# Kernel tuning notes

Hardware: AMD Instinct MI355X
Metric: run time of the kernel (lower is better)

The kernel has to match this reference:

```python
import jax, jax.numpy as jnp
import numpy as np
from jax import lax

RENDER_SIZE = (228, 304)   # (H, W) from __init__ default
FAR = 100.0                # z-buffer init, matches depth_map fill in source
EPS = 1e-7
CHUNK = 128                # faces processed per scan step


def setup_inputs() -> dict:
    key = jax.random.key(0)
    k1, k2, k3 = jax.random.split(key, 3)
    B, N, M = 1, 8192, 2048
    H, W = RENDER_SIZE
    uv = jax.random.uniform(k1, (B, N, 2), dtype=jnp.float32)           # u,v in [0,1]
    d = jax.random.uniform(k2, (B, N, 1), dtype=jnp.float32) * 4.0 + 1.0  # depth in [1,5]
    verts = jnp.concatenate([uv, d], axis=-1)                            # [B,N,3] depthmap format
    faces = jax.random.randint(k3, (B, M, 3), 0, N)                      # [B,M,3]
    fx = fy = 260.0
    K = jnp.array([[fx, 0.0, W / 2.0], [0.0, fy, H / 2.0], [0.0, 0.0, 1.0]], jnp.float32)
    intrinsics = jnp.tile(K[None], (B, 1, 1))
    ang = 0.02  # small camera rotation about y
    R = jnp.array([[np.cos(ang), 0.0, np.sin(ang)], [0.0, 1.0, 0.0],
                   [-np.sin(ang), 0.0, np.cos(ang)]], jnp.float32)
    R_mat = jnp.tile(R[None], (B, 1, 1))
    t_mat = jnp.tile(jnp.array([[0.01], [0.0], [0.02]], jnp.float32)[None], (B, 1, 1))
    return {"verts": verts, "faces": faces, "intrinsics": intrinsics,
            "R_mat": R_mat, "t_mat": t_mat}


def _convert_depthmap_to_cam(verts, K, H, W):
    # depthmap (u,v,d) -> camera coords; mirrors convert_depthmap_to_cam
    d = verts[..., 2:3]
    pix = jnp.concatenate([verts[..., 0:1] * W, verts[..., 1:2] * H,
                           jnp.ones_like(d)], axis=-1)                   # [B,N,3]
    Kinv = jnp.linalg.inv(K)
    return jnp.einsum('bij,bnj->bni', Kinv, pix) * d


def _project_cam_to_depthmap(cam, K, H, W):
    # camera coords -> depthmap (u,v,z); mirrors project_cam_to_depthmap
    z = cam[..., 2]
    p = jnp.stack([cam[..., 0] / (z + EPS), cam[..., 1] / (z + EPS),
                   jnp.ones_like(z)], axis=-1)
    p = jnp.einsum('bnj,bij->bni', p, K)  # matmul(p, K^T)
    u = jnp.clip(p[..., 0] / W, 0.0, 1.0)
    v = jnp.clip(p[..., 1] / H, 0.0, 1.0)
    return jnp.stack([u, v, z], axis=-1)


def _transform_depthmap(verts, K, R, t, H, W):
    cam = _convert_depthmap_to_cam(verts, K, H, W)                       # [B,N,3]
    cam2 = jnp.einsum('bij,bnj->bni', R, cam) + t[:, :, 0][:, None, :]   # R@x + t
    return _project_cam_to_depthmap(cam2, K, H, W)


def _rasterize(face_verts, S):
    """face_verts: [B,M,3,3] NDC (x,y) + depth z. Returns depth [B,S,S], sil [B,S,S]."""
    B, M = face_verts.shape[0], face_verts.shape[1]
    p = (2.0 * jnp.arange(S, dtype=face_verts.dtype) + 1.0 - S) / S      # NR pixel centers
    XP = p[None, None, None, :]   # x varies along last axis
    YP = p[None, None, :, None]   # y varies along rows

    chunks = face_verts.reshape(B, M // CHUNK, CHUNK, 3, 3).transpose(1, 0, 2, 3, 4)

    def step(carry, fvc):  # fvc: [B,C,3,3]
        depth, sil = carry
        x = fvc[..., 0][..., None, None]  # [B,C,3,1,1]
        y = fvc[..., 1][..., None, None]
        z = fvc[..., 2][..., None, None]
        x0, x1, x2 = x[:, :, 0], x[:, :, 1], x[:, :, 2]
        y0, y1, y2 = y[:, :, 0], y[:, :, 1], y[:, :, 2]
        z0, z1, z2 = z[:, :, 0], z[:, :, 1], z[:, :, 2]
        denom = (y1 - y2) * (x0 - x2) + (x2 - x1) * (y0 - y2)
        ok = jnp.abs(denom) > 1e-10
        safe = jnp.where(ok, denom, 1.0)
        w0 = ((y1 - y2) * (XP - x2) + (x2 - x1) * (YP - y2)) / safe      # [B,C,S,S]
        w1 = ((y2 - y0) * (XP - x2) + (x0 - x2) * (YP - y2)) / safe
        w2 = 1.0 - w0 - w1
        inside = (w0 >= 0) & (w1 >= 0) & (w2 >= 0) & ok
        inv_z = w0 / z0 + w1 / z1 + w2 / z2  # perspective-correct depth interp
        zp = 1.0 / jnp.where(jnp.abs(inv_z) > EPS, inv_z, EPS)
        zc = jnp.where(inside & (zp > 0), zp, FAR)
        depth = jnp.minimum(depth, zc.min(axis=1))                       # z-buffer update
        sil = jnp.maximum(sil, inside.any(axis=1).astype(depth.dtype))
        return (depth, sil), None

    init = (jnp.full((B, S, S), FAR, face_verts.dtype),
            jnp.zeros((B, S, S), face_verts.dtype))
    (depth, sil), _ = lax.scan(step, init, chunks)
    return depth, sil


def reference(verts, faces, intrinsics, R_mat, t_mat):
    H, W = RENDER_SIZE
    S = max(H, W)
    v = _transform_depthmap(verts, intrinsics, R_mat, t_mat, H, W)       # reprojected depthmap
    # depthmap [0,1] -> NDC [-1,1], keeping aspect via img_max_size
    ndc = jnp.concatenate([v[:, :, :1] * W / S * 2.0 - 1.0,
                           v[:, :, 1:2] * H / S * 2.0 - 1.0,
                           v[:, :, 2:]], axis=2)
    fv = jax.vmap(lambda vb, fb: vb[fb])(ndc, faces)                     # [B,M,3,3]
    depth, sil = _rasterize(fv, S)
    depth = depth[:, ::-1, :][:, :H, :W]  # flip(dim=1) then crop, as in _render
    sil = sil[:, ::-1, :][:, :H, :W]
    return jnp.stack([depth, sil], axis=1)  # [B,2,H,W]: depth + silhouette
```

## Files before the change

### kernel.cpp

```cpp
#include <hip/hip_runtime.h>

#define SS 304
#define HH 228
#define WW 304
#define FARV 100.0f
#define EPSV 1e-07f
#define SPLIT 16
#define CH 128

__device__ __forceinline__ void xform_vertex(
    float u, float v, float d,
    float fx, float cx, float fy, float cy,
    float r00, float r01, float r02,
    float r10, float r11, float r12,
    float r20, float r21, float r22,
    float t0, float t1, float t2,
    float& xn, float& yn, float& z)
{
#pragma clang fp contract(off)
    float ki00 = 1.0f / fx;
    float ki02 = -(cx / fx);
    float ki11 = 1.0f / fy;
    float ki12 = -(cy / fy);
    float px = u * (float)WW;
    float py = v * (float)HH;
    float c0 = (ki00 * px + ki02) * d;
    float c1 = (ki11 * py + ki12) * d;
    float c2 = d;
    float e0 = ((r00*c0 + r01*c1) + r02*c2) + t0;
    float e1 = ((r10*c0 + r11*c1) + r12*c2) + t1;
    float e2 = ((r20*c0 + r21*c1) + r22*c2) + t2;
    z = e2;
    float zd = z + EPSV;
    float p0 = e0 / zd;
    float p1 = e1 / zd;
    float q0 = p0 * fx + cx;
    float q1 = p1 * fy + cy;
    float uu = q0 / (float)WW; uu = fminf(fmaxf(uu, 0.0f), 1.0f);
    float vv = q1 / (float)HH; vv = fminf(fmaxf(vv, 0.0f), 1.0f);
    xn = uu * (float)WW / (float)SS * 2.0f - 1.0f;
    yn = vv * (float)HH / (float)SS * 2.0f - 1.0f;
}

__global__ __launch_bounds__(256) void prep_kernel(
    const float* __restrict__ verts,
    const int* __restrict__ faces,
    const float* __restrict__ Km,
    const float* __restrict__ Rm,
    const float* __restrict__ tm,
    float4* __restrict__ bboxArr,
    float4* __restrict__ G0arr,
    float4* __restrict__ G1arr,
    float2* __restrict__ G2arr,
    float* __restrict__ out, int M)
{
#pragma clang fp contract(off)
    int g = blockIdx.x * blockDim.x + threadIdx.x;
    if (g < HH * WW) {
        out[g] = FARV;
        out[HH * WW + g] = 0.0f;
    }
    if (g >= M) return;
    int m = g;
    int i0 = faces[3*m+0], i1 = faces[3*m+1], i2 = faces[3*m+2];
    float fx = Km[0], cx = Km[2], fy = Km[4], cy = Km[5];
    float r00 = Rm[0], r01 = Rm[1], r02 = Rm[2];
    float r10 = Rm[3], r11 = Rm[4], r12 = Rm[5];
    float r20 = Rm[6], r21 = Rm[7], r22 = Rm[8];
    float t0 = tm[0], t1 = tm[1], t2 = tm[2];

    float x0, y0, z0, x1, y1, z1, x2, y2, z2;
    xform_vertex(verts[3*i0+0], verts[3*i0+1], verts[3*i0+2], fx,cx,fy,cy,
                 r00,r01,r02,r10,r11,r12,r20,r21,r22,t0,t1,t2, x0,y0,z0);
    xform_vertex(verts[3*i1+0], verts[3*i1+1], verts[3*i1+2], fx,cx,fy,cy,
                 r00,r01,r02,r10,r11,r12,r20,r21,r22,t0,t1,t2, x1,y1,z1);
    xform_vertex(verts[3*i2+0], verts[3*i2+1], verts[3*i2+2], fx,cx,fy,cy,
                 r00,r01,r02,r10,r11,r12,r20,r21,r22,t0,t1,t2, x2,y2,z2);

    float A0 = y1 - y2;
    float B0 = x2 - x1;
    float A1 = y2 - y0;
    float B1 = x0 - x2;
    float dy02 = y0 - y2;
    float denom = A0 * B1 + B0 * dy02;
    bool ok = fabsf(denom) > 1e-10f;

    float xmin, xmax, ymin, ymax;
    if (ok) {
        xmin = fminf(x0, fminf(x1, x2)) - 1e-4f;
        xmax = fmaxf(x0, fmaxf(x1, x2)) + 1e-4f;
        ymin = fminf(y0, fminf(y1, y2)) - 1e-4f;
        ymax = fmaxf(y0, fmaxf(y1, y2)) + 1e-4f;
    } else {
        xmin = 1e30f; xmax = -1e30f; ymin = 1e30f; ymax = -1e30f;
    }
    bboxArr[m] = make_float4(xmin, xmax, ymin, ymax);

    float flip = (denom >= 0.0f) ? 1.0f : -1.0f;
    float sabs = fabsf(denom);
    float A0p = flip * A0, B0p = flip * B0;
    float C0p = -(A0p * x2 + B0p * y2);
    float A1p = flip * A1, B1p = flip * B1;
    float C1p = -(A1p * x2 + B1p * y2);
    float rz0 = 1.0f / z0, rz1 = 1.0f / z1, rz2 = 1.0f / z2;
    float D0 = rz0 / sabs, D1 = rz1 / sabs, D2 = rz2 / sabs;
    float d02 = D0 - D2, d12 = D1 - D2;
    float E = A0p * d02 + A1p * d12;
    float F = B0p * d02 + B1p * d12;
    float G = (C0p * d02 + C1p * d12) + sabs * D2;

    G0arr[m] = make_float4(A0p, B0p, C0p, sabs);
    G1arr[m] = make_float4(A1p, B1p, C1p, G);
    G2arr[m] = make_float2(E, F);
}

__global__ __launch_bounds__(256) void raster_kernel(
    const float4* __restrict__ bboxArr,
    const float4* __restrict__ G0arr,
    const float4* __restrict__ G1arr,
    const float2* __restrict__ G2arr,
    float* __restrict__ out, int M)
{
    __shared__ float4 sG0[CH];
    __shared__ float4 sG1[CH];
    __shared__ float2 sG2[CH];
    __shared__ int sCount;

    int tx = threadIdx.x, ty = threadIdx.y;
    int tid = ty * 16 + tx;
    int w = blockIdx.x * 16 + tx;
    int h = blockIdx.y * 16 + ty;

    int wlo = blockIdx.x * 16;
    int whi = min(wlo + 15, WW - 1);
    int hlo = blockIdx.y * 16;
    int hhi = min(hlo + 15, HH - 1);
    float txlo = ((float)(2*wlo + 1 - SS)) / (float)SS;
    float txhi = ((float)(2*whi + 1 - SS)) / (float)SS;
    float tylo = ((float)(2*(SS-1-hhi) + 1 - SS)) / (float)SS;
    float tyhi = ((float)(2*(SS-1-hlo) + 1 - SS)) / (float)SS;

    if (tid == 0) sCount = 0;
    __syncthreads();

    if (tid < CH) {
        int m = blockIdx.z * CH + tid;
        float4 rb = bboxArr[m];
        bool pass = !(rb.x > txhi || rb.y < txlo || rb.z > tyhi || rb.w < tylo);
        if (pass) {
            int i = atomicAdd(&sCount, 1);
            sG0[i] = G0arr[m];
            sG1[i] = G1arr[m];
            sG2[i] = G2arr[m];
        }
    }
    __syncthreads();
    int cnt = sCount;

    if (h < HH) {
        int irow = SS - 1 - h;
        float XP = ((float)(2*w    + 1 - SS)) / (float)SS;
        float YP = ((float)(2*irow + 1 - SS)) / (float)SS;

        float mx = 0.0f;

        for (int k = 0; k < cnt; ++k) {
            float4 g0 = sG0[k];
            float4 g1 = sG1[k];
            float2 g2 = sG2[k];
            float n0 = fmaf(g0.x, XP, fmaf(g0.y, YP, g0.z));
            float n1 = fmaf(g1.x, XP, fmaf(g1.y, YP, g1.z));
            float n2 = (g0.w - n0) - n1;
            float iz = fmaf(g2.x, XP, fmaf(g2.y, YP, g1.w));
            float m3 = fminf(fminf(n0, n1), n2);
            float cand = (m3 >= 0.0f) ? iz : 0.0f;
            mx = fmaxf(mx, cand);
        }

        if (mx > 0.0f) {
            float depth = __builtin_amdgcn_rcpf(mx);
            atomicMin((unsigned int*)&out[h * WW + w], __float_as_uint(depth));
            atomicMax((unsigned int*)&out[HH * WW + h * WW + w],
                      __float_as_uint(1.0f));
        }
    }
}

extern "C" void kernel_launch(void* const* d_in, const int* in_sizes, int n_in,
                              void* d_out, int out_size, void* d_ws, size_t ws_size,
                              hipStream_t stream) {
    const float* verts = (const float*)d_in[0];
    const int*   faces = (const int*)d_in[1];
    const float* K     = (const float*)d_in[2];
    const float* R     = (const float*)d_in[3];
    const float* t     = (const float*)d_in[4];
    float* out = (float*)d_out;

    int M = in_sizes[1] / 3;

    char* ws = (char*)d_ws;
    float4* bbox = (float4*)ws;                ws += (size_t)M * sizeof(float4);
    float4* G0   = (float4*)ws;                ws += (size_t)M * sizeof(float4);
    float4* G1   = (float4*)ws;                ws += (size_t)M * sizeof(float4);
    float2* G2   = (float2*)ws;                ws += (size_t)M * sizeof(float2);

    prep_kernel<<<(HH * WW + 255) / 256, 256, 0, stream>>>(
        verts, faces, K, R, t, bbox, G0, G1, G2, out, M);

    dim3 blk(16, 16);
    dim3 grd((WW + 15) / 16, (HH + 15) / 16, SPLIT);
    raster_kernel<<<grd, blk, 0, stream>>>(bbox, G0, G1, G2, out, M);
}
```

Measured before the change: 89.76 us.

## Rasterize two rows per thread and double faces per block chunk

Each thread now evaluates two pixels 16 rows apart, getting the second pixel's edge functions incrementally from the first with one FMA each. This amortizes the shared-memory face loads over two pixels. The face chunk grows to 256 with half as many splits, so all 256 threads take part in culling, and an M bound check is added. The trade-off is a bounding box twice as tall, so more faces pass culling per tile and more lanes can go idle, plus fewer blocks in the grid, which lowers occupancy.

```diff
diff --git a/kernel.cpp b/kernel.cpp
--- a/kernel.cpp
+++ b/kernel.cpp
@@ -5,8 +5,9 @@
 #define WW 304
 #define FARV 100.0f
 #define EPSV 1e-07f
-#define SPLIT 16
-#define CH 128
+#define SPLIT 8
+#define CH 256
+#define DYC (-32.0f / (float)SS)
 
 __device__ __forceinline__ void xform_vertex(
     float u, float v, float d,
@@ -128,13 +129,14 @@
 
     int tx = threadIdx.x, ty = threadIdx.y;
     int tid = ty * 16 + tx;
-    int w = blockIdx.x * 16 + tx;
-    int h = blockIdx.y * 16 + ty;
+    int w  = blockIdx.x * 16 + tx;
+    int h0 = blockIdx.y * 32 + ty;
+    int h1 = h0 + 16;
 
     int wlo = blockIdx.x * 16;
     int whi = min(wlo + 15, WW - 1);
-    int hlo = blockIdx.y * 16;
-    int hhi = min(hlo + 15, HH - 1);
+    int hlo = blockIdx.y * 32;
+    int hhi = min(hlo + 31, HH - 1);
     float txlo = ((float)(2*wlo + 1 - SS)) / (float)SS;
     float txhi = ((float)(2*whi + 1 - SS)) / (float)SS;
     float tylo = ((float)(2*(SS-1-hhi) + 1 - SS)) / (float)SS;
@@ -143,26 +145,29 @@
     if (tid == 0) sCount = 0;
     __syncthreads();
 
-    if (tid < CH) {
+    {
         int m = blockIdx.z * CH + tid;
-        float4 rb = bboxArr[m];
-        bool pass = !(rb.x > txhi || rb.y < txlo || rb.z > tyhi || rb.w < tylo);
-        if (pass) {
-            int i = atomicAdd(&sCount, 1);
-            sG0[i] = G0arr[m];
-            sG1[i] = G1arr[m];
-            sG2[i] = G2arr[m];
+        if (m < M) {
+            float4 rb = bboxArr[m];
+            bool pass = !(rb.x > txhi || rb.y < txlo || rb.z > tyhi || rb.w < tylo);
+            if (pass) {
+                int i = atomicAdd(&sCount, 1);
+                sG0[i] = G0arr[m];
+                sG1[i] = G1arr[m];
+                sG2[i] = G2arr[m];
+            }
         }
     }
     __syncthreads();
     int cnt = sCount;
 
-    if (h < HH) {
-        int irow = SS - 1 - h;
+    {
+        int irow = SS - 1 - h0;
         float XP = ((float)(2*w    + 1 - SS)) / (float)SS;
         float YP = ((float)(2*irow + 1 - SS)) / (float)SS;
 
-        float mx = 0.0f;
+        float mx0 = 0.0f;
+        float mx1 = 0.0f;
 
         for (int k = 0; k < cnt; ++k) {
             float4 g0 = sG0[k];
@@ -170,17 +175,28 @@
             float2 g2 = sG2[k];
             float n0 = fmaf(g0.x, XP, fmaf(g0.y, YP, g0.z));
             float n1 = fmaf(g1.x, XP, fmaf(g1.y, YP, g1.z));
+            float iz = fmaf(g2.x, XP, fmaf(g2.y, YP, g1.w));
             float n2 = (g0.w - n0) - n1;
-            float iz = fmaf(g2.x, XP, fmaf(g2.y, YP, g1.w));
             float m3 = fminf(fminf(n0, n1), n2);
-            float cand = (m3 >= 0.0f) ? iz : 0.0f;
-            mx = fmaxf(mx, cand);
-        }
-
-        if (mx > 0.0f) {
-            float depth = __builtin_amdgcn_rcpf(mx);
-            atomicMin((unsigned int*)&out[h * WW + w], __float_as_uint(depth));
-            atomicMax((unsigned int*)&out[HH * WW + h * WW + w],
+            mx0 = fmaxf(mx0, (m3 >= 0.0f) ? iz : 0.0f);
+            float n0b = fmaf(g0.y, DYC, n0);
+            float n1b = fmaf(g1.y, DYC, n1);
+            float izb = fmaf(g2.y, DYC, iz);
+            float n2b = (g0.w - n0b) - n1b;
+            float m3b = fminf(fminf(n0b, n1b), n2b);
+            mx1 = fmaxf(mx1, (m3b >= 0.0f) ? izb : 0.0f);
+        }
+
+        if (h0 < HH && mx0 > 0.0f) {
+            float depth = __builtin_amdgcn_rcpf(mx0);
+            atomicMin((unsigned int*)&out[h0 * WW + w], __float_as_uint(depth));
+            atomicMax((unsigned int*)&out[HH * WW + h0 * WW + w],
+                      __float_as_uint(1.0f));
+        }
+        if (h1 < HH && mx1 > 0.0f) {
+            float depth = __builtin_amdgcn_rcpf(mx1);
+            atomicMin((unsigned int*)&out[h1 * WW + w], __float_as_uint(depth));
+            atomicMax((unsigned int*)&out[HH * WW + h1 * WW + w],
                       __float_as_uint(1.0f));
         }
     }
@@ -208,6 +224,6 @@
         verts, faces, K, R, t, bbox, G0, G1, G2, out, M);
 
     dim3 blk(16, 16);
-    dim3 grd((WW + 15) / 16, (HH + 15) / 16, SPLIT);
+    dim3 grd((WW + 15) / 16, (HH + 31) / 32, SPLIT);
     raster_kernel<<<grd, blk, 0, stream>>>(bbox, G0, G1, G2, out, M);
 }
```

Result: faster. 81.38 us (-9.3%).

## Replace face-split raster grid with per-tile full loop, double-buffered staging

Applied to the files above, without the earlier changes.

Each 16x16 pixel tile now loops over all faces in batches of 256 instead of splitting faces across 16 z-blocks, so each pixel is written once directly and the global atomics and output init pass go away. Face culling adds an exact edge-function test against the tile corners, and compaction uses wave ballot plus one shared atomic per wave. Shared staging is double-buffered so the next batch is culled while the current one is rasterized. In exchange the grid shrinks to about 285 blocks, which lowers parallelism on a large GPU, and each block now does serial work over every face.

```diff
diff --git a/kernel.cpp b/kernel.cpp
--- a/kernel.cpp
+++ b/kernel.cpp
@@ -5,8 +5,6 @@
 #define WW 304
 #define FARV 100.0f
 #define EPSV 1e-07f
-#define SPLIT 16
-#define CH 128
 
 __device__ __forceinline__ void xform_vertex(
     float u, float v, float d,
@@ -51,17 +49,11 @@
     float4* __restrict__ bboxArr,
     float4* __restrict__ G0arr,
     float4* __restrict__ G1arr,
-    float2* __restrict__ G2arr,
-    float* __restrict__ out, int M)
+    float2* __restrict__ G2arr, int M)
 {
 #pragma clang fp contract(off)
-    int g = blockIdx.x * blockDim.x + threadIdx.x;
-    if (g < HH * WW) {
-        out[g] = FARV;
-        out[HH * WW + g] = 0.0f;
-    }
-    if (g >= M) return;
-    int m = g;
+    int m = blockIdx.x * blockDim.x + threadIdx.x;
+    if (m >= M) return;
     int i0 = faces[3*m+0], i1 = faces[3*m+1], i2 = faces[3*m+2];
     float fx = Km[0], cx = Km[2], fy = Km[4], cy = Km[5];
     float r00 = Rm[0], r01 = Rm[1], r02 = Rm[2];
@@ -121,68 +113,95 @@
     const float2* __restrict__ G2arr,
     float* __restrict__ out, int M)
 {
-    __shared__ float4 sG0[CH];
-    __shared__ float4 sG1[CH];
-    __shared__ float2 sG2[CH];
-    __shared__ int sCount;
-
-    int tx = threadIdx.x, ty = threadIdx.y;
-    int tid = ty * 16 + tx;
-    int w = blockIdx.x * 16 + tx;
-    int h = blockIdx.y * 16 + ty;
-
-    int wlo = blockIdx.x * 16;
-    int whi = min(wlo + 15, WW - 1);
-    int hlo = blockIdx.y * 16;
-    int hhi = min(hlo + 15, HH - 1);
-    float txlo = ((float)(2*wlo + 1 - SS)) / (float)SS;
-    float txhi = ((float)(2*whi + 1 - SS)) / (float)SS;
-    float tylo = ((float)(2*(SS-1-hhi) + 1 - SS)) / (float)SS;
-    float tyhi = ((float)(2*(SS-1-hlo) + 1 - SS)) / (float)SS;
-
-    if (tid == 0) sCount = 0;
+    __shared__ float4 sG0[2][256];
+    __shared__ float4 sG1[2][256];
+    __shared__ float2 sG2[2][256];
+    __shared__ int sCnt[2];
+
+    const int tx = threadIdx.x, ty = threadIdx.y;
+    const int tid = ty * 16 + tx;
+    const int w = blockIdx.x * 16 + tx;
+    const int h = blockIdx.y * 16 + ty;
+
+    const int wlo = blockIdx.x * 16, whi = wlo + 15;
+    const int hlo = blockIdx.y * 16, hhi = min(hlo + 15, HH - 1);
+    const float txlo = ((float)(2*wlo + 1 - SS)) / (float)SS;
+    const float txhi = ((float)(2*whi + 1 - SS)) / (float)SS;
+    const float tylo = ((float)(2*(SS-1-hhi) + 1 - SS)) / (float)SS;
+    const float tyhi = ((float)(2*(SS-1-hlo) + 1 - SS)) / (float)SS;
+
+    const int lane = tid & 63;
+    const unsigned long long lanes_below = (1ull << lane) - 1ull;
+
+    auto stage = [&](int b, int slot) {
+        int m = b * 256 + tid;
+        bool pass = false;
+        float4 g0, g1;
+        if (m < M) {
+            float4 rb = bboxArr[m];
+            if (!(rb.x > txhi || rb.y < txlo || rb.z > tyhi || rb.w < tylo)) {
+                g0 = G0arr[m];
+                g1 = G1arr[m];
+                float e0 = fmaxf(g0.x * txlo, g0.x * txhi)
+                         + fmaxf(g0.y * tylo, g0.y * tyhi) + g0.z;
+                float e1 = fmaxf(g1.x * txlo, g1.x * txhi)
+                         + fmaxf(g1.y * tylo, g1.y * tyhi) + g1.z;
+                float A2 = -(g0.x + g1.x);
+                float B2 = -(g0.y + g1.y);
+                float C2 = g0.w - g0.z - g1.z;
+                float e2 = fmaxf(A2 * txlo, A2 * txhi)
+                         + fmaxf(B2 * tylo, B2 * tyhi) + C2;
+                pass = (e0 >= -1e-5f) && (e1 >= -1e-5f) && (e2 >= -1e-5f);
+            }
+        }
+        unsigned long long mask = __ballot(pass);
+        int wtotal = __popcll(mask);
+        int wbase = 0;
+        if (lane == 0 && wtotal > 0) wbase = atomicAdd(&sCnt[slot], wtotal);
+        wbase = __shfl(wbase, 0);
+        if (pass) {
+            int i = wbase + (int)__popcll(mask & lanes_below);
+            sG0[slot][i] = g0;
+            sG1[slot][i] = g1;
+            sG2[slot][i] = G2arr[m];
+        }
+    };
+
+    if (tid < 2) sCnt[tid] = 0;
     __syncthreads();
-
-    if (tid < CH) {
-        int m = blockIdx.z * CH + tid;
-        float4 rb = bboxArr[m];
-        bool pass = !(rb.x > txhi || rb.y < txlo || rb.z > tyhi || rb.w < tylo);
-        if (pass) {
-            int i = atomicAdd(&sCount, 1);
-            sG0[i] = G0arr[m];
-            sG1[i] = G1arr[m];
-            sG2[i] = G2arr[m];
+    stage(0, 0);
+
+    const int irow = SS - 1 - h;
+    const float XP = ((float)(2*w    + 1 - SS)) / (float)SS;
+    const float YP = ((float)(2*irow + 1 - SS)) / (float)SS;
+    float mx = 0.0f;
+
+    const int nb = (M + 255) >> 8;
+    for (int b = 0; b < nb; ++b) {
+        int cur = b & 1, nxt = cur ^ 1;
+        __syncthreads();
+        int cnt = sCnt[cur];
+        __syncthreads();
+        if (tid == 0) sCnt[cur] = 0;
+        if (b + 1 < nb) stage(b + 1, nxt);
+        for (int k = 0; k < cnt; ++k) {
+            float4 g0 = sG0[cur][k];
+            float4 g1 = sG1[cur][k];
+            float2 g2 = sG2[cur][k];
+            float n0 = fmaf(g0.x, XP, fmaf(g0.y, YP, g0.z));
+            float n1 = fmaf(g1.x, XP, fmaf(g1.y, YP, g1.z));
+            float iz = fmaf(g2.x, XP, fmaf(g2.y, YP, g1.w));
+            float n2 = (g0.w - n0) - n1;
+            float m3 = fminf(fminf(n0, n1), n2);
+            mx = fmaxf(mx, (m3 >= 0.0f) ? iz : 0.0f);
         }
     }
-    __syncthreads();
-    int cnt = sCount;
 
     if (h < HH) {
-        int irow = SS - 1 - h;
-        float XP = ((float)(2*w    + 1 - SS)) / (float)SS;
-        float YP = ((float)(2*irow + 1 - SS)) / (float)SS;
-
-        float mx = 0.0f;
-
-        for (int k = 0; k < cnt; ++k) {
-            float4 g0 = sG0[k];
-            float4 g1 = sG1[k];
-            float2 g2 = sG2[k];
-            float n0 = fmaf(g0.x, XP, fmaf(g0.y, YP, g0.z));
-            float n1 = fmaf(g1.x, XP, fmaf(g1.y, YP, g1.z));
-            float n2 = (g0.w - n0) - n1;
-            float iz = fmaf(g2.x, XP, fmaf(g2.y, YP, g1.w));
-            float m3 = fminf(fminf(n0, n1), n2);
-            float cand = (m3 >= 0.0f) ? iz : 0.0f;
-            mx = fmaxf(mx, cand);
-        }
-
-        if (mx > 0.0f) {
-            float depth = __builtin_amdgcn_rcpf(mx);
-            atomicMin((unsigned int*)&out[h * WW + w], __float_as_uint(depth));
-            atomicMax((unsigned int*)&out[HH * WW + h * WW + w],
-                      __float_as_uint(1.0f));
-        }
+        bool cov = mx > 0.0f;
+        float depth = cov ? __builtin_amdgcn_rcpf(mx) : FARV;
+        out[h * WW + w] = depth;
+        out[HH * WW + h * WW + w] = cov ? 1.0f : 0.0f;
     }
 }
 
@@ -204,10 +223,10 @@
     float4* G1   = (float4*)ws;                ws += (size_t)M * sizeof(float4);
     float2* G2   = (float2*)ws;                ws += (size_t)M * sizeof(float2);
 
-    prep_kernel<<<(HH * WW + 255) / 256, 256, 0, stream>>>(
-        verts, faces, K, R, t, bbox, G0, G1, G2, out, M);
+    prep_kernel<<<(M + 255) / 256, 256, 0, stream>>>(
+        verts, faces, K, R, t, bbox, G0, G1, G2, M);
 
     dim3 blk(16, 16);
-    dim3 grd((WW + 15) / 16, (HH + 15) / 16, SPLIT);
+    dim3 grd(WW / 16, (HH + 15) / 16);
     raster_kernel<<<grd, blk, 0, stream>>>(bbox, G0, G1, G2, out, M);
 }
```

Result: slower. 132.3 us (+47.4%).
